# Optimization experiments

Measured on AMD Instinct MI355X. Metric: run time of the kernel, lower is better.

## Reference

```python
import jax, jax.numpy as jnp
import numpy as np
import math

N = 3072      # number of graph nodes
D = 256       # in_dim == out_dim
H = 8         # heads
EPS = 1e-5    # LayerNorm eps (torch default)


def _glorot(key, shape):
    fan = shape[-2] + shape[-1]
    std = math.sqrt(6.0 / fan)
    return jax.random.uniform(key, shape, jnp.float32, -std, std)


def layer_norm(x, g, b):
    mu = jnp.mean(x, axis=-1, keepdims=True)
    var = jnp.mean(jnp.square(x - mu), axis=-1, keepdims=True)
    return (x - mu) * jax.lax.rsqrt(var + EPS) * g + b


def setup_inputs() -> dict:
    key = jax.random.key(0)
    ks = jax.random.split(key, 12)
    input_x = jax.random.normal(ks[0], (N, D), jnp.float32)
    # degrees: positive floats in [1, 50)
    deg = 1.0 + 49.0 * jax.random.uniform(ks[1], (N,), jnp.float32)
    WQ = _glorot(ks[2], (H, D, D))
    WK = _glorot(ks[3], (H, D, D))
    WV = _glorot(ks[4], (H, D, D))
    # linears stored as [in, out] (math-equivalent to torch's [out,in] transposed)
    lin_attn_w = _glorot(ks[5], (H * D, D)); lin_attn_b = jnp.zeros((D,), jnp.float32)
    lin_w = _glorot(ks[6], (2 * D, D));       lin_b = jnp.zeros((D,), jnp.float32)
    fnn1_w = _glorot(ks[7], (D, D));          fnn1_b = jnp.zeros((D,), jnp.float32)
    fnn2_w = _glorot(ks[8], (D, D));          fnn2_b = jnp.zeros((D,), jnp.float32)
    ln1_g = jnp.ones((D,), jnp.float32); ln1_b = jnp.zeros((D,), jnp.float32)
    ln2_g = jnp.ones((D,), jnp.float32); ln2_b = jnp.zeros((D,), jnp.float32)
    return dict(input_x=input_x, deg=deg, WQ=WQ, WK=WK, WV=WV,
                lin_attn_w=lin_attn_w, lin_attn_b=lin_attn_b,
                lin_w=lin_w, lin_b=lin_b,
                ln1_g=ln1_g, ln1_b=ln1_b,
                fnn1_w=fnn1_w, fnn1_b=fnn1_b,
                fnn2_w=fnn2_w, fnn2_b=fnn2_b,
                ln2_g=ln2_g, ln2_b=ln2_b)


def reference(input_x, deg, WQ, WK, WV, lin_attn_w, lin_attn_b,
              lin_w, lin_b, ln1_g, ln1_b, fnn1_w, fnn1_b,
              fnn2_w, fnn2_b, ln2_g, ln2_b):
    n = input_x.shape[0]
    # --- multi-head attention over all nodes ---
    Q = jnp.einsum('nd,hde->hne', input_x, WQ)   # [H,N,D]
    K = jnp.einsum('nd,hde->hne', input_x, WK)
    V = jnp.einsum('nd,hde->hne', input_x, WV)
    scores = jnp.einsum('hne,hme->hnm', Q, K)    # [H,N,N]
    # diagonal self-mask: QKT[i] += diag_embed(diag(QKT[i]) - 1e20)
    idx = jnp.arange(n)
    diag_vals = scores[:, idx, idx]
    scores = scores.at[:, idx, idx].add(diag_vals - 1e20)
    attn = jax.nn.softmax(scores / math.sqrt(D), axis=-1)
    attn_x = jnp.einsum('hnm,hme->hne', attn, V)           # [H,N,D]
    attn_cat = jnp.transpose(attn_x, (1, 0, 2)).reshape(n, H * D)
    attn_out = attn_cat @ lin_attn_w + lin_attn_b          # [N,D]
    # --- degree-norm concat + residual + LN ---
    x1 = jnp.concatenate([input_x, attn_out / jnp.sqrt(deg)[:, None]], axis=-1)
    x1 = x1 @ lin_w + lin_b
    x1 = layer_norm(input_x + x1, ln1_g, ln1_b)
    # --- FFN block (dropout inactive at eval) ---
    x2 = jax.nn.relu(x1 @ fnn1_w + fnn1_b)
    x2 = x2 @ fnn2_w + fnn2_b
    return layer_norm(x1 + x2, ln2_g, ln2_b)
```

## Files before the change

kernel.cpp:

```cpp
#include <hip/hip_runtime.h>
#include <hip/hip_bf16.h>
#include <stdint.h>

typedef __bf16 bf16x8_t __attribute__((ext_vector_type(8)));
typedef short  s16x8_t  __attribute__((ext_vector_type(8)));
typedef unsigned short u16x4_t __attribute__((ext_vector_type(4)));
typedef float  f32x4_t __attribute__((ext_vector_type(4)));

#define NTOK 3072
#define NHEAD 8
#define NSPLIT 4

__device__ __forceinline__ unsigned short f2bf(float f) {
  union { float f; uint32_t u; } v; v.f = f;
  uint32_t r = v.u + 0x7fffu + ((v.u >> 16) & 1u);
  return (unsigned short)(r >> 16);
}
__device__ __forceinline__ float bf2f(unsigned short s) {
  union { uint32_t u; float f; } v; v.u = ((uint32_t)s) << 16;
  return v.f;
}

__device__ __forceinline__ void gload_lds16(const void* g, void* lds) {
  __builtin_amdgcn_global_load_lds(
      (const __attribute__((address_space(1))) uint32_t*)g,
      (__attribute__((address_space(3))) uint32_t*)lds, 16, 0, 0);
}

template <int CTRL>
__device__ __forceinline__ float dpp_mv(float x) {
  union { float f; int i; } u; u.f = x;
  u.i = __builtin_amdgcn_update_dpp(0, u.i, CTRL, 0xf, 0xf, true);
  return u.f;
}
__device__ __forceinline__ float red_max16(float x) {
  x = fmaxf(x, dpp_mv<0xB1>(x));
  x = fmaxf(x, dpp_mv<0x4E>(x));
  x = fmaxf(x, dpp_mv<0x141>(x));
  x = fmaxf(x, dpp_mv<0x140>(x));
  return x;
}
__device__ __forceinline__ float red_sum16(float x) {
  x += dpp_mv<0xB1>(x);
  x += dpp_mv<0x4E>(x);
  x += dpp_mv<0x141>(x);
  x += dpp_mv<0x140>(x);
  return x;
}

__global__ void prep_all(const float* __restrict__ WQ, const float* __restrict__ WK,
                         const float* __restrict__ WV, const float* __restrict__ law,
                         const float* __restrict__ lw, const float* __restrict__ f1w,
                         const float* __restrict__ f2w, const float* __restrict__ x,
                         unsigned short* __restrict__ qkvwT, unsigned short* __restrict__ lawT,
                         unsigned short* __restrict__ lwT, unsigned short* __restrict__ f1T,
                         unsigned short* __restrict__ f2T, unsigned short* __restrict__ xa) {
  __shared__ float tile[64][65];
  const int id = blockIdx.x;
  const int t = threadIdx.x;
  if (id >= 576) {
    int n0 = (id - 576) * 64;
    int col = (t & 63) * 4;
#pragma unroll
    for (int i = 0; i < 16; ++i) {
      int n = n0 + i * 4 + (t >> 6);
      f32x4_t v = *(const f32x4_t*)(x + (size_t)n * 256 + col);
      u16x4_t o;
#pragma unroll
      for (int j = 0; j < 4; ++j) o[j] = f2bf(v[j]);
      *(u16x4_t*)(xa + (size_t)n * 512 + col) = o;
    }
    return;
  }
  const float* src; unsigned short* dst; int sld, dld, d0, e0;
  if (id < 384) {
    int z = id >> 4, tl = id & 15;
    int op = z >> 3, hh = z & 7;
    src = ((op == 0) ? WQ : (op == 1) ? WK : WV) + (size_t)hh * 65536;
    dst = qkvwT + (size_t)z * 65536;
    sld = 256; dld = 256; d0 = (tl >> 2) * 64; e0 = (tl & 3) * 64;
  } else if (id < 512) {
    int tl = id - 384;
    src = law; dst = lawT; sld = 256; dld = 2048;
    d0 = (tl >> 2) * 64; e0 = (tl & 3) * 64;
  } else if (id < 544) {
    int tl = id - 512;
    src = lw; dst = lwT; sld = 256; dld = 512;
    d0 = (tl >> 2) * 64; e0 = (tl & 3) * 64;
  } else if (id < 560) {
    int tl = id - 544;
    src = f1w; dst = f1T; sld = 256; dld = 256;
    d0 = (tl >> 2) * 64; e0 = (tl & 3) * 64;
  } else {
    int tl = id - 560;
    src = f2w; dst = f2T; sld = 256; dld = 256;
    d0 = (tl >> 2) * 64; e0 = (tl & 3) * 64;
  }
  int tr = t >> 4, tc4 = (t & 15) * 4;
#pragma unroll
  for (int i = 0; i < 4; ++i) {
    int d = i * 16 + tr;
    f32x4_t v = *(const f32x4_t*)(src + (size_t)(d0 + d) * sld + e0 + tc4);
    tile[d][tc4] = v[0]; tile[d][tc4 + 1] = v[1]; tile[d][tc4 + 2] = v[2]; tile[d][tc4 + 3] = v[3];
  }
  __syncthreads();
#pragma unroll
  for (int i = 0; i < 4; ++i) {
    int e = i * 16 + tr;
    u16x4_t o;
#pragma unroll
    for (int j = 0; j < 4; ++j) o[j] = f2bf(tile[tc4 + j][e]);
    *(u16x4_t*)(dst + (size_t)(e0 + e) * dld + d0 + tc4) = o;
  }
}

template <int BM, int BN>
__global__ __launch_bounds__(256, 2) void gemm_kernel(
    const unsigned short* __restrict__ A, int lda,
    const unsigned short* __restrict__ B, int ldb,
    void* __restrict__ Cout, int ldc, int Klen,
    const float* __restrict__ bias,
    const float* __restrict__ resid, int ldr,
    const float* __restrict__ deg, int flags,
    float* __restrict__ part, long pstride) {
  constexpr int WM = BM / 2, WN = BN / 2, FM = WM / 16, FN = WN / 16;
  __shared__ unsigned short As[BM * 32];
  __shared__ unsigned short Bs[BN * 32];
  const int t = threadIdx.x;
  const int w = t >> 6, l = t & 63;
  const int l15 = l & 15, lhi = l >> 4;
  const int row0 = blockIdx.y * BM, col0 = blockIdx.x * BN;
  const int wr = (w >> 1) * WM, wc = (w & 1) * WN;

  f32x4_t acc[FM][FN];
#pragma unroll
  for (int m = 0; m < FM; ++m)
#pragma unroll
    for (int n = 0; n < FN; ++n) acc[m][n] = (f32x4_t){0.f, 0.f, 0.f, 0.f};

  const int srow = l >> 2;
  const int spc  = (l & 3) * 16;
  const int kofs0 = blockIdx.z * Klen;
  const int nkt = Klen >> 5;
  for (int kt = 0; kt < nkt; ++kt) {
    const int koff = kofs0 + kt * 32;
    __syncthreads();
#pragma unroll
    for (int c = w; c < BM / 16; c += 4) {
      int ar = c * 16 + srow;
      int lcb = spc ^ (((ar >> 1) & 3) << 4);
      gload_lds16(A + (size_t)(row0 + ar) * lda + koff + (lcb >> 1), &As[c * 512]);
    }
#pragma unroll
    for (int c = w; c < BN / 16; c += 4) {
      int br = c * 16 + srow;
      int lcb = spc ^ (((br >> 1) & 3) << 4);
      gload_lds16(B + (size_t)(col0 + br) * ldb + koff + (lcb >> 1), &Bs[c * 512]);
    }
    __syncthreads();
    bf16x8_t af[FM], bfr[FN];
#pragma unroll
    for (int m = 0; m < FM; ++m) {
      int ar = wr + m * 16 + l15;
      af[m] = *(const bf16x8_t*)(&As[(ar * 64 + ((lhi * 16) ^ (((ar >> 1) & 3) << 4))) >> 1]);
    }
#pragma unroll
    for (int n = 0; n < FN; ++n) {
      int br = wc + n * 16 + l15;
      bfr[n] = *(const bf16x8_t*)(&Bs[(br * 64 + ((lhi * 16) ^ (((br >> 1) & 3) << 4))) >> 1]);
    }
#pragma unroll
    for (int m = 0; m < FM; ++m)
#pragma unroll
      for (int n = 0; n < FN; ++n)
        acc[m][n] = __builtin_amdgcn_mfma_f32_16x16x32_bf16(af[m], bfr[n], acc[m][n], 0, 0, 0);
  }

  const bool relu = flags & 1, obf = flags & 2, dsc = flags & 4, ppart = flags & 8;
#pragma unroll
  for (int m = 0; m < FM; ++m) {
#pragma unroll
    for (int r = 0; r < 4; ++r) {
      int grow = row0 + wr + m * 16 + lhi * 4 + r;
      float sc = dsc ? rsqrtf(deg[grow]) : 1.0f;
#pragma unroll
      for (int n = 0; n < FN; ++n) {
        int gcol = col0 + wc + n * 16 + l15;
        float v = acc[m][n][r];
        if (ppart) {
          part[(size_t)blockIdx.z * pstride + (size_t)grow * ldc + gcol] = v;
          continue;
        }
        if (bias) v += bias[gcol];
        v *= sc;
        if (resid) v += resid[(size_t)grow * ldr + gcol];
        if (relu) v = fmaxf(v, 0.f);
        if (obf)
          ((unsigned short*)Cout)[(size_t)grow * ldc + gcol] = f2bf(v);
        else
          ((float*)Cout)[(size_t)grow * ldc + gcol] = v;
      }
    }
  }
}

__global__ void attn_reduce(const float* __restrict__ part, const float* __restrict__ lab,
                            const float* __restrict__ deg, unsigned short* __restrict__ xa) {
  int n = blockIdx.x, d = threadIdx.x;
  float s = 0.f;
#pragma unroll
  for (int z = 0; z < 4; ++z) s += part[((size_t)z * NTOK + n) * 256 + d];
  xa[(size_t)n * 512 + 256 + d] = f2bf((s + lab[d]) * rsqrtf(deg[n]));
}

#define VSW(e) ((((((e) >> 1) & 3) ^ (((e) >> 3) & 3))) << 4)
__global__ __launch_bounds__(256, 2) void flash_kernel(
    const unsigned short* __restrict__ qkv, unsigned short* __restrict__ pO,
    float* __restrict__ ml) {
  __shared__ unsigned short Ks[32 * 256];
  __shared__ unsigned short Vt[256 * 32];
  __shared__ unsigned short Ps[4][16 * 32];
  const int bid = blockIdx.x;
  const int hs = bid % (NHEAD * NSPLIT);
  const int qb = bid / (NHEAD * NSPLIT);
  const int h = hs / NSPLIT;
  const int split = hs % NSPLIT;
  const int q0 = qb * 64;
  const int t = threadIdx.x, w = t >> 6, l = t & 63;
  const int l15 = l & 15, lhi = l >> 4;

  const int vn0 = (t & 7) * 4;
  const int ve0 = (t >> 3) * 8;

  bf16x8_t qf[8];
  {
    const unsigned short* Qb = qkv + (size_t)(q0 + w * 16 + l15) * 6144 + h * 256 + lhi * 8;
#pragma unroll
    for (int kk = 0; kk < 8; ++kk) qf[kk] = *(const bf16x8_t*)(Qb + kk * 32);
  }
  f32x4_t o[16];
#pragma unroll
  for (int et = 0; et < 16; ++et) o[et] = (f32x4_t){0.f, 0.f, 0.f, 0.f};
  float m_run[4] = {-1e30f, -1e30f, -1e30f, -1e30f};
  float l_run[4] = {0.f, 0.f, 0.f, 0.f};

  const int nt0 = split * (96 / NSPLIT), nt1 = nt0 + 96 / NSPLIT;
  for (int nt = nt0; nt < nt1; ++nt) {
    const int kv0 = nt * 32;
    __syncthreads();
    {
      int rh = l >> 5;
      int pc = (l & 31) * 16;
#pragma unroll
      for (int i = 0; i < 4; ++i) {
        int c = w * 4 + i;
        int kr = c * 2 + rh;
        int lcb = pc ^ ((kr & 7) << 4);
        gload_lds16(qkv + (size_t)(kv0 + kr) * 6144 + 2048 + h * 256 + (lcb >> 1), &Ks[c * 512]);
      }
    }
    {
      s16x8_t rv[4];
      const unsigned short* Vg = qkv + (size_t)(kv0 + vn0) * 6144 + 4096 + h * 256 + ve0;
#pragma unroll
      for (int rr = 0; rr < 4; ++rr) rv[rr] = *(const s16x8_t*)(Vg + rr * 6144);
#pragma unroll
      for (int j = 0; j < 8; ++j) {
        int e = ve0 + j;
        uint64_t pk = (uint64_t)(unsigned short)rv[0][j] |
                      ((uint64_t)(unsigned short)rv[1][j] << 16) |
                      ((uint64_t)(unsigned short)rv[2][j] << 32) |
                      ((uint64_t)(unsigned short)rv[3][j] << 48);
        int pb = e * 64 + ((vn0 * 2) ^ VSW(e));
        *(uint64_t*)(&Vt[pb >> 1]) = pk;
      }
    }
    __syncthreads();

    f32x4_t s[2];
#pragma unroll
    for (int ni = 0; ni < 2; ++ni) s[ni] = (f32x4_t){0.f, 0.f, 0.f, 0.f};
    __builtin_amdgcn_s_setprio(1);
#pragma unroll
    for (int kk = 0; kk < 8; ++kk) {
#pragma unroll
      for (int ni = 0; ni < 2; ++ni) {
        int br = ni * 16 + l15;
        bf16x8_t kb = *(const bf16x8_t*)(&Ks[(br * 512 + ((kk * 64 + lhi * 16) ^ ((br & 7) << 4))) >> 1]);
        s[ni] = __builtin_amdgcn_mfma_f32_16x16x32_bf16(qf[kk], kb, s[ni], 0, 0, 0);
      }
    }
    __builtin_amdgcn_s_setprio(0);

    float p[2][4];
    float alpha[4];
#pragma unroll
    for (int r = 0; r < 4; ++r) {
      int grow = q0 + w * 16 + lhi * 4 + r;
      float sv0 = s[0][r] * 0.0625f;
      float sv1 = s[1][r] * 0.0625f;
      if (kv0 + l15 == grow) sv0 = -1e30f;
      if (kv0 + 16 + l15 == grow) sv1 = -1e30f;
      float mx = red_max16(fmaxf(sv0, sv1));
      float mn = fmaxf(m_run[r], mx);
      alpha[r] = __expf(m_run[r] - mn);
      m_run[r] = mn;
      float pv0 = __expf(sv0 - mn);
      float pv1 = __expf(sv1 - mn);
      p[0][r] = pv0; p[1][r] = pv1;
      float ls = red_sum16(pv0 + pv1);
      l_run[r] = l_run[r] * alpha[r] + ls;
    }
#pragma unroll
    for (int et = 0; et < 16; ++et)
#pragma unroll
      for (int r = 0; r < 4; ++r) o[et][r] *= alpha[r];

    unsigned short* Pw = &Ps[w][0];
#pragma unroll
    for (int ni = 0; ni < 2; ++ni)
#pragma unroll
      for (int r = 0; r < 4; ++r) {
        int prow = lhi * 4 + r;
        int pb = prow * 64 + ((((ni * 16 + l15) * 2)) ^ (((prow >> 1) & 3) << 4));
        Pw[pb >> 1] = f2bf(p[ni][r]);
      }
    bf16x8_t pa = *(const bf16x8_t*)(&Pw[(l15 * 64 + ((lhi * 16) ^ (((l15 >> 1) & 3) << 4))) >> 1]);
    __builtin_amdgcn_s_setprio(1);
#pragma unroll
    for (int et = 0; et < 16; ++et) {
      int er = et * 16 + l15;
      bf16x8_t vb = *(const bf16x8_t*)(&Vt[(er * 64 + ((lhi * 16) ^ VSW(er))) >> 1]);
      o[et] = __builtin_amdgcn_mfma_f32_16x16x32_bf16(pa, vb, o[et], 0, 0, 0);
    }
    __builtin_amdgcn_s_setprio(0);
  }

  const size_t sh = (size_t)(split * NHEAD + h);
#pragma unroll
  for (int et = 0; et < 16; ++et)
#pragma unroll
    for (int r = 0; r < 4; ++r) {
      int grow = q0 + w * 16 + lhi * 4 + r;
      pO[(sh * NTOK + grow) * 256 + et * 16 + l15] = f2bf(o[et][r]);
    }
  if (l15 == 0) {
#pragma unroll
    for (int r = 0; r < 4; ++r) {
      int grow = q0 + w * 16 + lhi * 4 + r;
      ml[(sh * NTOK + grow) * 2] = m_run[r];
      ml[(sh * NTOK + grow) * 2 + 1] = l_run[r];
    }
  }
}

__global__ void flash_combine(const unsigned short* __restrict__ pO,
                              const float* __restrict__ ml,
                              unsigned short* __restrict__ acat) {
  int n = blockIdx.x, t = threadIdx.x;
  int h = t >> 5, e0 = (t & 31) * 8;
  float ms[NSPLIT], ls[NSPLIT];
  float M = -1e30f;
#pragma unroll
  for (int s = 0; s < NSPLIT; ++s) {
    size_t b = ((size_t)(s * NHEAD + h) * NTOK + n) * 2;
    ms[s] = ml[b]; ls[s] = ml[b + 1];
    M = fmaxf(M, ms[s]);
  }
  float den = 0.f;
  float num[8];
#pragma unroll
  for (int j = 0; j < 8; ++j) num[j] = 0.f;
#pragma unroll
  for (int s = 0; s < NSPLIT; ++s) {
    float ws = __expf(ms[s] - M);
    den += ws * ls[s];
    s16x8_t ov = *(const s16x8_t*)(pO + ((size_t)(s * NHEAD + h) * NTOK + n) * 256 + e0);
#pragma unroll
    for (int j = 0; j < 8; ++j) num[j] += ws * bf2f((unsigned short)ov[j]);
  }
  float rden = 1.0f / den;
  s16x8_t out;
#pragma unroll
  for (int j = 0; j < 8; ++j) out[j] = (short)f2bf(num[j] * rden);
  *(s16x8_t*)(acat + (size_t)n * 2048 + h * 256 + e0) = out;
}

__global__ __launch_bounds__(256, 2) void tail_fused(
    const unsigned short* __restrict__ xa, const unsigned short* __restrict__ lwT,
    const unsigned short* __restrict__ f1T, const unsigned short* __restrict__ f2T,
    const float* __restrict__ x, const float* __restrict__ lb,
    const float* __restrict__ ln1g, const float* __restrict__ ln1b,
    const float* __restrict__ f1b, const float* __restrict__ f2b,
    const float* __restrict__ ln2g, const float* __restrict__ ln2b,
    float* __restrict__ out) {
  __shared__ unsigned short As[16 * 32];
  __shared__ unsigned short Bs[256 * 32];
  __shared__ unsigned short Xs[16 * 256];
  __shared__ float red[16][4][2];
  const int t = threadIdx.x, w = t >> 6, l = t & 63;
  const int l15 = l & 15, lhi = l >> 4;
  const int row0 = blockIdx.x * 16;
  const int wc = w * 64;
  const int srow = l >> 2, spc = (l & 3) * 16;

  f32x4_t acc[4];
#pragma unroll
  for (int n = 0; n < 4; ++n) acc[n] = (f32x4_t){0.f, 0.f, 0.f, 0.f};
  for (int kt = 0; kt < 16; ++kt) {
    __syncthreads();
    if (w == 0) {
      int ar = srow;
      int lcb = spc ^ (((ar >> 1) & 3) << 4);
      gload_lds16(xa + (size_t)(row0 + ar) * 512 + kt * 32 + (lcb >> 1), &As[0]);
    }
#pragma unroll
    for (int c = w; c < 16; c += 4) {
      int br = c * 16 + srow;
      int lcb = spc ^ (((br >> 1) & 3) << 4);
      gload_lds16(lwT + (size_t)br * 512 + kt * 32 + (lcb >> 1), &Bs[c * 512]);
    }
    __syncthreads();
    bf16x8_t af = *(const bf16x8_t*)(&As[(l15 * 64 + ((lhi * 16) ^ (((l15 >> 1) & 3) << 4))) >> 1]);
#pragma unroll
    for (int n = 0; n < 4; ++n) {
      int br = wc + n * 16 + l15;
      bf16x8_t bfr = *(const bf16x8_t*)(&Bs[(br * 64 + ((lhi * 16) ^ (((br >> 1) & 3) << 4))) >> 1]);
      acc[n] = __builtin_amdgcn_mfma_f32_16x16x32_bf16(af, bfr, acc[n], 0, 0, 0);
    }
  }
  float x1v[4][4];
#pragma unroll
  for (int r = 0; r < 4; ++r) {
    int grow = row0 + lhi * 4 + r;
#pragma unroll
    for (int n = 0; n < 4; ++n) {
      int col = wc + n * 16 + l15;
      x1v[n][r] = acc[n][r] + lb[col] + x[(size_t)grow * 256 + col];
    }
  }
#pragma unroll
  for (int r = 0; r < 4; ++r) {
    float s = x1v[0][r] + x1v[1][r] + x1v[2][r] + x1v[3][r];
    float q = x1v[0][r] * x1v[0][r] + x1v[1][r] * x1v[1][r] +
              x1v[2][r] * x1v[2][r] + x1v[3][r] * x1v[3][r];
    s = red_sum16(s); q = red_sum16(q);
    if (l15 == 0) { red[lhi * 4 + r][w][0] = s; red[lhi * 4 + r][w][1] = q; }
  }
  __syncthreads();
#pragma unroll
  for (int r = 0; r < 4; ++r) {
    int row = lhi * 4 + r;
    float s = red[row][0][0] + red[row][1][0] + red[row][2][0] + red[row][3][0];
    float q = red[row][0][1] + red[row][1][1] + red[row][2][1] + red[row][3][1];
    float mu = s * (1.0f / 256.0f);
    float var = q * (1.0f / 256.0f) - mu * mu;
    float rstd = rsqrtf(var + 1e-5f);
#pragma unroll
    for (int n = 0; n < 4; ++n) {
      int col = wc + n * 16 + l15;
      float xv = (x1v[n][r] - mu) * rstd * ln1g[col] + ln1b[col];
      x1v[n][r] = xv;
      int pb = row * 512 + ((col * 2) ^ ((row & 7) << 4));
      Xs[pb >> 1] = f2bf(xv);
    }
  }

  f32x4_t acc2[4];
#pragma unroll
  for (int n = 0; n < 4; ++n) acc2[n] = (f32x4_t){0.f, 0.f, 0.f, 0.f};
  for (int kt = 0; kt < 8; ++kt) {
    __syncthreads();
#pragma unroll
    for (int c = w; c < 16; c += 4) {
      int br = c * 16 + srow;
      int lcb = spc ^ (((br >> 1) & 3) << 4);
      gload_lds16(f1T + (size_t)br * 256 + kt * 32 + (lcb >> 1), &Bs[c * 512]);
    }
    __syncthreads();
    bf16x8_t af = *(const bf16x8_t*)(&Xs[(l15 * 512 + (((kt * 32 + lhi * 8) * 2) ^ ((l15 & 7) << 4))) >> 1]);
#pragma unroll
    for (int n = 0; n < 4; ++n) {
      int br = wc + n * 16 + l15;
      bf16x8_t bfr = *(const bf16x8_t*)(&Bs[(br * 64 + ((lhi * 16) ^ (((br >> 1) & 3) << 4))) >> 1]);
      acc2[n] = __builtin_amdgcn_mfma_f32_16x16x32_bf16(af, bfr, acc2[n], 0, 0, 0);
    }
  }
  __syncthreads();
#pragma unroll
  for (int r = 0; r < 4; ++r) {
    int row = lhi * 4 + r;
#pragma unroll
    for (int n = 0; n < 4; ++n) {
      int col = wc + n * 16 + l15;
      float v = fmaxf(acc2[n][r] + f1b[col], 0.f);
      int pb = row * 512 + ((col * 2) ^ ((row & 7) << 4));
      Xs[pb >> 1] = f2bf(v);
    }
  }

  f32x4_t acc3[4];
#pragma unroll
  for (int n = 0; n < 4; ++n) acc3[n] = (f32x4_t){0.f, 0.f, 0.f, 0.f};
  for (int kt = 0; kt < 8; ++kt) {
    __syncthreads();
#pragma unroll
    for (int c = w; c < 16; c += 4) {
      int br = c * 16 + srow;
      int lcb = spc ^ (((br >> 1) & 3) << 4);
      gload_lds16(f2T + (size_t)br * 256 + kt * 32 + (lcb >> 1), &Bs[c * 512]);
    }
    __syncthreads();
    bf16x8_t af = *(const bf16x8_t*)(&Xs[(l15 * 512 + (((kt * 32 + lhi * 8) * 2) ^ ((l15 & 7) << 4))) >> 1]);
#pragma unroll
    for (int n = 0; n < 4; ++n) {
      int br = wc + n * 16 + l15;
      bf16x8_t bfr = *(const bf16x8_t*)(&Bs[(br * 64 + ((lhi * 16) ^ (((br >> 1) & 3) << 4))) >> 1]);
      acc3[n] = __builtin_amdgcn_mfma_f32_16x16x32_bf16(af, bfr, acc3[n], 0, 0, 0);
    }
  }
  float u2v[4][4];
#pragma unroll
  for (int r = 0; r < 4; ++r) {
#pragma unroll
    for (int n = 0; n < 4; ++n) {
      int col = wc + n * 16 + l15;
      u2v[n][r] = acc3[n][r] + f2b[col] + x1v[n][r];
    }
  }
  __syncthreads();
#pragma unroll
  for (int r = 0; r < 4; ++r) {
    float s = u2v[0][r] + u2v[1][r] + u2v[2][r] + u2v[3][r];
    float q = u2v[0][r] * u2v[0][r] + u2v[1][r] * u2v[1][r] +
              u2v[2][r] * u2v[2][r] + u2v[3][r] * u2v[3][r];
    s = red_sum16(s); q = red_sum16(q);
    if (l15 == 0) { red[lhi * 4 + r][w][0] = s; red[lhi * 4 + r][w][1] = q; }
  }
  __syncthreads();
#pragma unroll
  for (int r = 0; r < 4; ++r) {
    int row = lhi * 4 + r;
    int grow = row0 + row;
    float s = red[row][0][0] + red[row][1][0] + red[row][2][0] + red[row][3][0];
    float q = red[row][0][1] + red[row][1][1] + red[row][2][1] + red[row][3][1];
    float mu = s * (1.0f / 256.0f);
    float var = q * (1.0f / 256.0f) - mu * mu;
    float rstd = rsqrtf(var + 1e-5f);
#pragma unroll
    for (int n = 0; n < 4; ++n) {
      int col = wc + n * 16 + l15;
      out[(size_t)grow * 256 + col] = (u2v[n][r] - mu) * rstd * ln2g[col] + ln2b[col];
    }
  }
}

extern "C" void kernel_launch(void* const* d_in, const int* in_sizes, int n_in,
                              void* d_out, int out_size, void* d_ws, size_t ws_size,
                              hipStream_t stream) {
  const float* x    = (const float*)d_in[0];
  const float* deg  = (const float*)d_in[1];
  const float* WQ   = (const float*)d_in[2];
  const float* WK   = (const float*)d_in[3];
  const float* WV   = (const float*)d_in[4];
  const float* law  = (const float*)d_in[5];
  const float* lab  = (const float*)d_in[6];
  const float* lw   = (const float*)d_in[7];
  const float* lb   = (const float*)d_in[8];
  const float* ln1g = (const float*)d_in[9];
  const float* ln1b = (const float*)d_in[10];
  const float* f1w  = (const float*)d_in[11];
  const float* f1b  = (const float*)d_in[12];
  const float* f2w  = (const float*)d_in[13];
  const float* f2b  = (const float*)d_in[14];
  const float* ln2g = (const float*)d_in[15];
  const float* ln2b = (const float*)d_in[16];

  char* ws = (char*)d_ws;
  size_t off = 0;
  auto alloc = [&](size_t bytes) {
    void* p = ws + off;
    off += (bytes + 255) & ~(size_t)255;
    return p;
  };
  unsigned short* qkvwT = (unsigned short*)alloc((size_t)6144 * 256 * 2);
  unsigned short* lawT  = (unsigned short*)alloc((size_t)256 * 2048 * 2);
  unsigned short* lwT   = (unsigned short*)alloc((size_t)256 * 512 * 2);
  unsigned short* f1T   = (unsigned short*)alloc((size_t)256 * 256 * 2);
  unsigned short* f2T   = (unsigned short*)alloc((size_t)256 * 256 * 2);
  unsigned short* xa    = (unsigned short*)alloc((size_t)NTOK * 512 * 2);
  unsigned short* qkv   = (unsigned short*)alloc((size_t)NTOK * 6144 * 2);
  unsigned short* acat  = (unsigned short*)alloc((size_t)NTOK * 2048 * 2);
  unsigned short* pO    = (unsigned short*)alloc((size_t)NSPLIT * NHEAD * NTOK * 256 * 2);
  float*          mlp   = (float*)alloc((size_t)NSPLIT * NHEAD * NTOK * 2 * 4);
  float*          apart = (float*)alloc((size_t)4 * NTOK * 256 * 4);

  prep_all<<<624, 256, 0, stream>>>(WQ, WK, WV, law, lw, f1w, f2w, x,
                                    qkvwT, lawT, lwT, f1T, f2T, xa);

  gemm_kernel<128, 128><<<dim3(48, 24), 256, 0, stream>>>(
      xa, 512, qkvwT, 256, qkv, 6144, 256, nullptr, nullptr, 0, nullptr, 2, nullptr, 0);

  flash_kernel<<<NTOK / 64 * NHEAD * NSPLIT, 256, 0, stream>>>(qkv, pO, mlp);
  flash_combine<<<NTOK, 256, 0, stream>>>(pO, mlp, acat);

  gemm_kernel<64, 64><<<dim3(4, 48, 4), 256, 0, stream>>>(
      acat, 2048, lawT, 2048, nullptr, 256, 512, nullptr, nullptr, 0, nullptr, 8,
      apart, (long)NTOK * 256);
  attn_reduce<<<NTOK, 256, 0, stream>>>(apart, lab, deg, xa);

  tail_fused<<<NTOK / 16, 256, 0, stream>>>(
      xa, lwT, f1T, f2T, x, lb, ln1g, ln1b, f1b, f2b, ln2g, ln2b, (float*)d_out);
}
```

Measured before the change: 362.4 us.

## Double flash-attention KV tile from 32 to 64 keys per iteration

Each iteration of the flash kernel now processes 64 keys instead of 32, so K, V-transpose and P buffers in shared memory double and the swizzles are rewritten for the wider rows. This halves the number of barriers, online-softmax rescales of the 16 output accumulators, and cross-lane reductions per key. It also issues twice as many MFMAs between syncs. The cost is doubled LDS use (about 66 KB per block), which may limit the two-blocks-per-CU occupancy target, plus extra registers for the wider V staging and score tiles.

```diff
diff --git a/kernel.cpp b/kernel.cpp
--- a/kernel.cpp
+++ b/kernel.cpp
@@ -5,6 +5,7 @@
 typedef __bf16 bf16x8_t __attribute__((ext_vector_type(8)));
 typedef short  s16x8_t  __attribute__((ext_vector_type(8)));
 typedef unsigned short u16x4_t __attribute__((ext_vector_type(4)));
+typedef unsigned short u16x8_t __attribute__((ext_vector_type(8)));
 typedef float  f32x4_t __attribute__((ext_vector_type(4)));
 
 #define NTOK 3072
@@ -213,13 +214,14 @@
   xa[(size_t)n * 512 + 256 + d] = f2bf((s + lab[d]) * rsqrtf(deg[n]));
 }
 
-#define VSW(e) ((((((e) >> 1) & 3) ^ (((e) >> 3) & 3))) << 4)
+#define VSW64(e) (((((e) & 7) ^ (((e) >> 3) & 7))) << 4)
+#define PSW(r)   (((r) & 7) << 4)
 __global__ __launch_bounds__(256, 2) void flash_kernel(
     const unsigned short* __restrict__ qkv, unsigned short* __restrict__ pO,
     float* __restrict__ ml) {
-  __shared__ unsigned short Ks[32 * 256];
-  __shared__ unsigned short Vt[256 * 32];
-  __shared__ unsigned short Ps[4][16 * 32];
+  __shared__ unsigned short Ks[64 * 256];
+  __shared__ unsigned short Vt[256 * 64];
+  __shared__ unsigned short Ps[4][16 * 64];
   const int bid = blockIdx.x;
   const int hs = bid % (NHEAD * NSPLIT);
   const int qb = bid / (NHEAD * NSPLIT);
@@ -229,7 +231,7 @@
   const int t = threadIdx.x, w = t >> 6, l = t & 63;
   const int l15 = l & 15, lhi = l >> 4;
 
-  const int vn0 = (t & 7) * 4;
+  const int vn0 = (t & 7) * 8;
   const int ve0 = (t >> 3) * 8;
 
   bf16x8_t qf[8];
@@ -244,47 +246,45 @@
   float m_run[4] = {-1e30f, -1e30f, -1e30f, -1e30f};
   float l_run[4] = {0.f, 0.f, 0.f, 0.f};
 
-  const int nt0 = split * (96 / NSPLIT), nt1 = nt0 + 96 / NSPLIT;
-  for (int nt = nt0; nt < nt1; ++nt) {
-    const int kv0 = nt * 32;
+  for (int it = 0; it < 12; ++it) {
+    const int kv0 = (split * 12 + it) * 64;
     __syncthreads();
     {
       int rh = l >> 5;
       int pc = (l & 31) * 16;
 #pragma unroll
-      for (int i = 0; i < 4; ++i) {
-        int c = w * 4 + i;
+      for (int i = 0; i < 8; ++i) {
+        int c = w * 8 + i;
         int kr = c * 2 + rh;
         int lcb = pc ^ ((kr & 7) << 4);
         gload_lds16(qkv + (size_t)(kv0 + kr) * 6144 + 2048 + h * 256 + (lcb >> 1), &Ks[c * 512]);
       }
     }
     {
-      s16x8_t rv[4];
+      s16x8_t rv[8];
       const unsigned short* Vg = qkv + (size_t)(kv0 + vn0) * 6144 + 4096 + h * 256 + ve0;
 #pragma unroll
-      for (int rr = 0; rr < 4; ++rr) rv[rr] = *(const s16x8_t*)(Vg + rr * 6144);
+      for (int rr = 0; rr < 8; ++rr) rv[rr] = *(const s16x8_t*)(Vg + rr * 6144);
 #pragma unroll
       for (int j = 0; j < 8; ++j) {
         int e = ve0 + j;
-        uint64_t pk = (uint64_t)(unsigned short)rv[0][j] |
-                      ((uint64_t)(unsigned short)rv[1][j] << 16) |
-                      ((uint64_t)(unsigned short)rv[2][j] << 32) |
-                      ((uint64_t)(unsigned short)rv[3][j] << 48);
-        int pb = e * 64 + ((vn0 * 2) ^ VSW(e));
-        *(uint64_t*)(&Vt[pb >> 1]) = pk;
+        u16x8_t pk;
+#pragma unroll
+        for (int rr = 0; rr < 8; ++rr) pk[rr] = (unsigned short)rv[rr][j];
+        int pb = e * 128 + ((vn0 * 2) ^ VSW64(e));
+        *(u16x8_t*)(&Vt[pb >> 1]) = pk;
       }
     }
     __syncthreads();
 
-    f32x4_t s[2];
-#pragma unroll
-    for (int ni = 0; ni < 2; ++ni) s[ni] = (f32x4_t){0.f, 0.f, 0.f, 0.f};
+    f32x4_t s[4];
+#pragma unroll
+    for (int ni = 0; ni < 4; ++ni) s[ni] = (f32x4_t){0.f, 0.f, 0.f, 0.f};
     __builtin_amdgcn_s_setprio(1);
 #pragma unroll
     for (int kk = 0; kk < 8; ++kk) {
 #pragma unroll
-      for (int ni = 0; ni < 2; ++ni) {
+      for (int ni = 0; ni < 4; ++ni) {
         int br = ni * 16 + l15;
         bf16x8_t kb = *(const bf16x8_t*)(&Ks[(br * 512 + ((kk * 64 + lhi * 16) ^ ((br & 7) << 4))) >> 1]);
         s[ni] = __builtin_amdgcn_mfma_f32_16x16x32_bf16(qf[kk], kb, s[ni], 0, 0, 0);
@@ -292,23 +292,32 @@
     }
     __builtin_amdgcn_s_setprio(0);
 
-    float p[2][4];
+    float p[4][4];
     float alpha[4];
 #pragma unroll
     for (int r = 0; r < 4; ++r) {
       int grow = q0 + w * 16 + lhi * 4 + r;
-      float sv0 = s[0][r] * 0.0625f;
-      float sv1 = s[1][r] * 0.0625f;
-      if (kv0 + l15 == grow) sv0 = -1e30f;
-      if (kv0 + 16 + l15 == grow) sv1 = -1e30f;
-      float mx = red_max16(fmaxf(sv0, sv1));
+      float sv[4];
+      float mx0 = -1e30f, mx1 = -1e30f;
+#pragma unroll
+      for (int ni = 0; ni < 4; ++ni) {
+        float x = s[ni][r] * 0.0625f;
+        if (kv0 + ni * 16 + l15 == grow) x = -1e30f;
+        sv[ni] = x;
+        if (ni & 1) mx1 = fmaxf(mx1, x); else mx0 = fmaxf(mx0, x);
+      }
+      float mx = red_max16(fmaxf(mx0, mx1));
       float mn = fmaxf(m_run[r], mx);
       alpha[r] = __expf(m_run[r] - mn);
       m_run[r] = mn;
-      float pv0 = __expf(sv0 - mn);
-      float pv1 = __expf(sv1 - mn);
-      p[0][r] = pv0; p[1][r] = pv1;
-      float ls = red_sum16(pv0 + pv1);
+      float ls = 0.f;
+#pragma unroll
+      for (int ni = 0; ni < 4; ++ni) {
+        float pv = __expf(sv[ni] - mn);
+        p[ni][r] = pv;
+        ls += pv;
+      }
+      ls = red_sum16(ls);
       l_run[r] = l_run[r] * alpha[r] + ls;
     }
 #pragma unroll
@@ -318,20 +327,23 @@
 
     unsigned short* Pw = &Ps[w][0];
 #pragma unroll
-    for (int ni = 0; ni < 2; ++ni)
+    for (int ni = 0; ni < 4; ++ni)
 #pragma unroll
       for (int r = 0; r < 4; ++r) {
         int prow = lhi * 4 + r;
-        int pb = prow * 64 + ((((ni * 16 + l15) * 2)) ^ (((prow >> 1) & 3) << 4));
+        int pb = prow * 128 + (((ni * 16 + l15) * 2) ^ PSW(prow));
         Pw[pb >> 1] = f2bf(p[ni][r]);
       }
-    bf16x8_t pa = *(const bf16x8_t*)(&Pw[(l15 * 64 + ((lhi * 16) ^ (((l15 >> 1) & 3) << 4))) >> 1]);
+    bf16x8_t pa0 = *(const bf16x8_t*)(&Pw[(l15 * 128 + ((lhi * 16) ^ PSW(l15))) >> 1]);
+    bf16x8_t pa1 = *(const bf16x8_t*)(&Pw[(l15 * 128 + ((64 + lhi * 16) ^ PSW(l15))) >> 1]);
     __builtin_amdgcn_s_setprio(1);
 #pragma unroll
     for (int et = 0; et < 16; ++et) {
       int er = et * 16 + l15;
-      bf16x8_t vb = *(const bf16x8_t*)(&Vt[(er * 64 + ((lhi * 16) ^ VSW(er))) >> 1]);
-      o[et] = __builtin_amdgcn_mfma_f32_16x16x32_bf16(pa, vb, o[et], 0, 0, 0);
+      bf16x8_t vb0 = *(const bf16x8_t*)(&Vt[(er * 128 + ((lhi * 16) ^ VSW64(er))) >> 1]);
+      bf16x8_t vb1 = *(const bf16x8_t*)(&Vt[(er * 128 + ((64 + lhi * 16) ^ VSW64(er))) >> 1]);
+      o[et] = __builtin_amdgcn_mfma_f32_16x16x32_bf16(pa0, vb0, o[et], 0, 0, 0);
+      o[et] = __builtin_amdgcn_mfma_f32_16x16x32_bf16(pa1, vb1, o[et], 0, 0, 0);
     }
     __builtin_amdgcn_s_setprio(0);
   }
```

Measured after the change: 324.8 us. 1.12x faster.
